# Kernel optimization log

Hardware: AMD Instinct MI355X
Metric: run time of the kernel (lower is better)

Reference implementation:

```python
import jax, jax.numpy as jnp
import numpy as np

VOCAB = 50000
EMB = 128
HID = 256
OUT = 1


def setup_inputs() -> dict:
    key = jax.random.key(0)
    ks = jax.random.split(key, 8)
    B, T = 256, 512
    s_emb = 1.0 / np.sqrt(EMB)
    s_hid = 1.0 / np.sqrt(HID)
    return {
        "x": jax.random.randint(ks[0], (B, T), 0, VOCAB, dtype=jnp.int32),
        "emb_table": jax.random.normal(ks[1], (VOCAB, EMB), dtype=jnp.float32),
        "W_ih": jax.random.uniform(ks[2], (4 * HID, EMB), jnp.float32, -s_hid, s_hid),
        "W_hh": jax.random.uniform(ks[3], (4 * HID, HID), jnp.float32, -s_hid, s_hid),
        "b_ih": jax.random.uniform(ks[4], (4 * HID,), jnp.float32, -s_hid, s_hid),
        "b_hh": jax.random.uniform(ks[5], (4 * HID,), jnp.float32, -s_hid, s_hid),
        "W_fc": jax.random.uniform(ks[6], (OUT, HID), jnp.float32, -s_hid, s_hid),
        "b_fc": jax.random.uniform(ks[7], (OUT,), jnp.float32, -s_hid, s_hid),
    }


def _lstm_last_hidden(embedded, W_ih, W_hh, b_ih, b_hh):
    # embedded: [B, T, E]; PyTorch gate order: i, f, g, o
    B = embedded.shape[0]
    H = W_hh.shape[1]
    # precompute input projections for all timesteps: [T, B, 4H]
    x_proj = jnp.einsum('bte,ge->tbg', embedded, W_ih) + b_ih + b_hh

    def step(carry, xp):
        h, c = carry
        gates = xp + h @ W_hh.T  # [B, 4H]
        i, f, g, o = jnp.split(gates, 4, axis=-1)
        i = jax.nn.sigmoid(i)
        f = jax.nn.sigmoid(f)
        g = jnp.tanh(g)
        o = jax.nn.sigmoid(o)
        c = f * c + i * g
        h = o * jnp.tanh(c)
        return (h, c), None

    h0 = jnp.zeros((B, H), embedded.dtype)
    c0 = jnp.zeros((B, H), embedded.dtype)
    (h_last, _), _ = jax.lax.scan(step, (h0, c0), x_proj)
    return h_last  # [B, H] == lstm_out[:, -1, :]


def reference(x, emb_table, W_ih, W_hh, b_ih, b_hh, W_fc, b_fc):
    embedded = emb_table[x]  # [B, T, E]
    h_last = _lstm_last_hidden(embedded, W_ih, W_hh, b_ih, b_hh)
    logits = h_last @ W_fc.T + b_fc  # [B, OUT]
    return jax.nn.sigmoid(logits)
```

## Files before the change

kernel.cpp:

```cpp
#include <hip/hip_runtime.h>
#include <hip/hip_bf16.h>
#include <stdint.h>

#define VOCAB 50000
#define EMB   128
#define HID   256
#define G4    1024
#define BATCH 256
#define SEQ   512
#define LOG2E 1.4426950408889634f

typedef __attribute__((ext_vector_type(8))) short bf16x8;
typedef __attribute__((ext_vector_type(4))) float f32x4;
typedef __attribute__((ext_vector_type(4))) int   i32x4;

__device__ __forceinline__ ushort f2bf(float f) {
  uint32_t u; __builtin_memcpy(&u, &f, 4);
  uint32_t r = (u + 0x7fffu + ((u >> 16) & 1u)) >> 16;
  return (ushort)r;
}
__device__ __forceinline__ float asf(uint32_t x) {
  float f; __builtin_memcpy(&f, &x, 4);
  return f;
}
__device__ __forceinline__ float rcp(float x) { return __builtin_amdgcn_rcpf(x); }
__device__ __forceinline__ float ex2(float x) { return __builtin_amdgcn_exp2f(x); }

#define WAIT_LGKM() asm volatile("s_waitcnt lgkmcnt(0)" ::: "memory")
#define RAW_BAR()  do { __builtin_amdgcn_sched_barrier(0); \
                        __builtin_amdgcn_s_barrier(); \
                        __builtin_amdgcn_sched_barrier(0); } while (0)

__global__ __launch_bounds__(256) void k_proj(
    const float* __restrict__ emb, const float* __restrict__ W_ih,
    const float* __restrict__ b_ih, const float* __restrict__ b_hh,
    ushort* __restrict__ proj) {
  const int lane = threadIdx.x & 63;
  const int wv = threadIdx.x >> 6;
  const int vbase = (blockIdx.x * 4 + wv) * 64;
  const int lm = lane & 15, lq = lane >> 4;
  const int nt0 = blockIdx.y * 32;

  bf16x8 A[4][4];
  #pragma unroll
  for (int mt = 0; mt < 4; ++mt) {
    int v = vbase + mt * 16 + lm;
    int vc = v < VOCAB ? v : 0;
    const float* rp = emb + (size_t)vc * EMB;
    #pragma unroll
    for (int kt = 0; kt < 4; ++kt) {
      const float* p = rp + kt * 32 + lq * 8;
      #pragma unroll
      for (int i = 0; i < 8; ++i) A[mt][kt][i] = (short)f2bf(p[i]);
    }
  }
  for (int ntl = 0; ntl < 32; ++ntl) {
    const int g = (nt0 + ntl) * 16 + lm;
    const int newcol = (g & 255) * 4 + (g >> 8);
    bf16x8 B[4];
    #pragma unroll
    for (int kt = 0; kt < 4; ++kt) {
      const float* p = W_ih + (size_t)g * EMB + kt * 32 + lq * 8;
      #pragma unroll
      for (int i = 0; i < 8; ++i) B[kt][i] = (short)f2bf(p[i]);
    }
    const float bias = b_ih[g] + b_hh[g];
    #pragma unroll
    for (int mt = 0; mt < 4; ++mt) {
      f32x4 acc = {0.f, 0.f, 0.f, 0.f};
      #pragma unroll
      for (int kt = 0; kt < 4; ++kt)
        acc = __builtin_amdgcn_mfma_f32_16x16x32_bf16(A[mt][kt], B[kt], acc, 0, 0, 0);
      #pragma unroll
      for (int r = 0; r < 4; ++r) {
        int row = vbase + mt * 16 + lq * 4 + r;
        if (row < VOCAB) proj[(size_t)row * G4 + newcol] = f2bf((acc[r] + bias) * LOG2E);
      }
    }
  }
}

__global__ __launch_bounds__(256) void k_w2(const float* __restrict__ Whh,
                                            int* __restrict__ W3) {
  const int t = blockIdx.x * 256 + threadIdx.x;
  const int lane = t & 63, c = t >> 6;
  const int kq = c & 15, wv = (c >> 4) & 7, v = c >> 7;
  const int gp = lane >> 5;
  const int j = wv * 32 + (lane & 31);
  const int g = gp * 2 + v;
  const float* src = Whh + (size_t)(g * 256 + j) * HID + kq * 16;
  unsigned d[4];
  #pragma unroll
  for (int e = 0; e < 4; ++e) {
    unsigned acc = 0;
    #pragma unroll
    for (int b = 0; b < 4; ++b) {
      int q = (int)rintf(src[e * 4 + b] * 2032.f);
      q = q > 127 ? 127 : (q < -127 ? -127 : q);
      acc |= ((unsigned)q & 0xffu) << (8 * b);
    }
    d[e] = acc;
  }
  i32x4 o = {(int)d[0], (int)d[1], (int)d[2], (int)d[3]};
  *(i32x4*)(W3 + (size_t)(c * 64 + lane) * 4) = o;
}

__global__ __launch_bounds__(512, 1) void k_lstm(
    const int* __restrict__ x, const ushort* __restrict__ proj,
    const int* __restrict__ W3, const float* __restrict__ W_fc,
    const float* __restrict__ b_fc, float* __restrict__ out) {
  __shared__ __align__(16) char hbuf[2][256];
  __shared__ __align__(16) int xlds[SEQ];
  __shared__ float red[8];

  const int tid = threadIdx.x;
  const int lane = tid & 63, wv = tid >> 6;
  const int gp = lane >> 5;
  const int j = wv * 32 + (lane & 31);
  const int b0 = blockIdx.x;
  const unsigned colb = (unsigned)(j * 4 + gp * 2) * 2u;

  i32x4 Wd0[16], Wd1[16];
  {
    const i32x4* wb = (const i32x4*)W3;
    #pragma unroll
    for (int kq = 0; kq < 16; ++kq) {
      Wd0[kq] = wb[(size_t)((0 * 8 + wv) * 16 + kq) * 64 + lane];
      Wd1[kq] = wb[(size_t)((1 * 8 + wv) * 16 + kq) * 64 + lane];
    }
    #pragma unroll
    for (int kq = 0; kq < 16; ++kq) {
      asm volatile("" : "+v"(Wd0[kq]));
      asm volatile("" : "+v"(Wd1[kq]));
    }
  }

  for (int i = tid; i < SEQ; i += 512) xlds[i] = x[b0 * SEQ + i];
  if (tid < 128) ((int*)hbuf)[tid] = 0;

  float c = 0.f, hl = 0.f;
  __syncthreads();

  const char* projb = (const char*)proj;
  unsigned xp0, xp1;
  xp0 = *(const unsigned*)(projb + (unsigned)xlds[0] * 2048u + colb);
  xp1 = *(const unsigned*)(projb + (unsigned)xlds[1] * 2048u + colb);

  const float S2 = LOG2E / 258064.f;

#define STEP(T, RB, WB, XP)                                                   \
  {                                                                           \
    int p0 = 0, p1 = 0, p2 = 0, p3 = 0;                    \
    int q0 = 0, q1 = 0, q2 = 0, q3 = 0;                    \
    _Pragma("unroll")                                                         \
    for (int kh = 0; kh < 2; ++kh) {                                          \
      i32x4 hq[8];                                                            \
      _Pragma("unroll")                                                       \
      for (int k8 = 0; k8 < 8; ++k8)                                          \
        hq[k8] = *(const i32x4*)(hbuf[RB] + (kh * 8 + k8) * 16);              \
      _Pragma("unroll")                                                       \
      for (int k8 = 0; k8 < 8; ++k8) {                                        \
        const int kq = kh * 8 + k8;                                           \
        p0 = __builtin_amdgcn_sdot4(hq[k8][0], Wd0[kq][0], p0, false);        \
        p1 = __builtin_amdgcn_sdot4(hq[k8][1], Wd0[kq][1], p1, false);        \
        p2 = __builtin_amdgcn_sdot4(hq[k8][2], Wd0[kq][2], p2, false);        \
        p3 = __builtin_amdgcn_sdot4(hq[k8][3], Wd0[kq][3], p3, false);        \
        q0 = __builtin_amdgcn_sdot4(hq[k8][0], Wd1[kq][0], q0, false);        \
        q1 = __builtin_amdgcn_sdot4(hq[k8][1], Wd1[kq][1], q1, false);        \
        q2 = __builtin_amdgcn_sdot4(hq[k8][2], Wd1[kq][2], q2, false);        \
        q3 = __builtin_amdgcn_sdot4(hq[k8][3], Wd1[kq][3], q3, false);        \
      }                                                                       \
    }                                                                         \
    int a0 = (p0 + p1) + (p2 + p3);                                           \
    int a1 = (q0 + q1) + (q2 + q3);                                           \
    float gv0 = (float)a0 * S2 + asf(XP << 16);                               \
    float gv1 = (float)a1 * S2 + asf(XP & 0xffff0000u);                       \
    float og0 = __shfl_xor(gv0, 32);                                          \
    float og1 = __shfl_xor(gv1, 32);                                          \
    float gi = gp ? og0 : gv0;                                                \
    float gf = gp ? og1 : gv1;                                                \
    float gg = gp ? gv0 : og0;                                                \
    float go = gp ? gv1 : og1;                                                \
    float si_ = rcp(1.f + ex2(-gi));                                          \
    float sf_ = rcp(1.f + ex2(-gf));                                          \
    float eg_ = ex2(gg + gg);                                                 \
    float tg_ = (eg_ - 1.f) * rcp(eg_ + 1.f);                                 \
    float so_ = rcp(1.f + ex2(-go));                                          \
    float cn_ = sf_ * c + si_ * tg_;                                          \
    c = cn_;                                                                  \
    float e2_ = ex2(cn_ * (2.f * LOG2E));                                     \
    float tc_ = 1.f - 2.f * rcp(e2_ + 1.f);                                   \
    float h_ = so_ * tc_;                                                     \
    hl = h_;                                                                  \
    if (gp == 0) hbuf[WB][j] = (char)(int)rintf(h_ * 127.f);                  \
    {                                                     \
      int t2_ = ((T) + 2 < SEQ) ? (T) + 2 : SEQ - 1;                          \
      XP = *(const unsigned*)(projb + (unsigned)xlds[t2_] * 2048u + colb);    \
    }                                                                         \
    WAIT_LGKM();                                                              \
    RAW_BAR();                                                                \
  }

  STEP(0, 0, 1, xp0);
  #pragma clang loop unroll(disable)
  for (int tt = 0; tt < 255; ++tt) {
    STEP(2 * tt + 1, 1, 0, xp1);
    STEP(2 * tt + 2, 0, 1, xp0);
  }
  STEP(511, 1, 0, xp1);

  float p = hl * W_fc[j];
  p += __shfl_xor(p, 1);
  p += __shfl_xor(p, 2);
  p += __shfl_xor(p, 4);
  p += __shfl_xor(p, 8);
  p += __shfl_xor(p, 16);
  if (lane == 0) red[wv] = p;
  __syncthreads();
  if (tid == 0) {
    float s = 0.f;
    #pragma unroll
    for (int w = 0; w < 8; ++w) s += red[w];
    s += b_fc[0];
    out[b0] = rcp(1.f + ex2(-s * LOG2E));
  }
}

extern "C" void kernel_launch(void* const* d_in, const int* in_sizes, int n_in,
                              void* d_out, int out_size, void* d_ws, size_t ws_size,
                              hipStream_t stream) {
  const int*   x    = (const int*)d_in[0];
  const float* emb  = (const float*)d_in[1];
  const float* W_ih = (const float*)d_in[2];
  const float* W_hh = (const float*)d_in[3];
  const float* b_ih = (const float*)d_in[4];
  const float* b_hh = (const float*)d_in[5];
  const float* W_fc = (const float*)d_in[6];
  const float* b_fc = (const float*)d_in[7];
  float* out = (float*)d_out;

  char* ws = (char*)d_ws;
  ushort* proj = (ushort*)ws;
  int*    W3   = (int*)(ws + 102400000);

  k_proj<<<dim3(196, 2), dim3(256), 0, stream>>>(emb, W_ih, b_ih, b_hh, proj);
  k_w2<<<dim3(64), dim3(256), 0, stream>>>(W_hh, W3);
  k_lstm<<<dim3(256), dim3(512), 0, stream>>>(x, proj, W3, W_fc, b_fc, out);
}
```

Baseline: 559.2 us.

## Split recurrent gate matvec between int8 MFMA and sdot4 paths

Gates g and o of the recurrent matvec now go through int8 MFMA (16x16x64) with weights held in AGPRs. Gates i and f stay on the sdot4 path, with K split across the two half-waves and combined by a shuffle. The W_hh quantization is split into two packing kernels with new layouts, and the projection load is widened to fetch all four gates per lane. The aim is to shorten the per-timestep serial dot-product latency by moving half the work onto the matrix cores. The cost is extra bpermutes and MFMA latency on the critical path, plus wasted MFMA rows because only one batch row is real.

```diff
diff --git a/kernel.cpp b/kernel.cpp
--- a/kernel.cpp
+++ b/kernel.cpp
@@ -13,6 +13,7 @@
 typedef __attribute__((ext_vector_type(8))) short bf16x8;
 typedef __attribute__((ext_vector_type(4))) float f32x4;
 typedef __attribute__((ext_vector_type(4))) int   i32x4;
+typedef __attribute__((ext_vector_type(2))) unsigned u32x2;
 
 __device__ __forceinline__ ushort f2bf(float f) {
   uint32_t u; __builtin_memcpy(&u, &f, 4);
@@ -81,14 +82,12 @@
 }
 
 __global__ __launch_bounds__(256) void k_w2(const float* __restrict__ Whh,
-                                            int* __restrict__ W3) {
+                                            int* __restrict__ W2) {
   const int t = blockIdx.x * 256 + threadIdx.x;
-  const int lane = t & 63, c = t >> 6;
-  const int kq = c & 15, wv = (c >> 4) & 7, v = c >> 7;
-  const int gp = lane >> 5;
-  const int j = wv * 32 + (lane & 31);
-  const int g = gp * 2 + v;
-  const float* src = Whh + (size_t)(g * 256 + j) * HID + kq * 16;
+  const int lane = t & 63, kc = (t >> 6) & 3, nt2 = (t >> 8) & 3, wv = (t >> 10) & 7;
+  const int grow = 512 + (nt2 >> 1) * 256 + wv * 32 + (nt2 & 1) * 16 + (lane & 15);
+  const int k0 = kc * 64 + (lane >> 4) * 16;
+  const float* src = Whh + (size_t)grow * HID + k0;
   unsigned d[4];
   #pragma unroll
   for (int e = 0; e < 4; ++e) {
@@ -102,37 +101,75 @@
     d[e] = acc;
   }
   i32x4 o = {(int)d[0], (int)d[1], (int)d[2], (int)d[3]};
-  *(i32x4*)(W3 + (size_t)(c * 64 + lane) * 4) = o;
+  *(i32x4*)(W2 + (size_t)t * 4) = o;
+}
+
+__global__ __launch_bounds__(256) void k_w3(const float* __restrict__ Whh,
+                                            int* __restrict__ W3) {
+  const int t = blockIdx.x * 256 + threadIdx.x;
+  const int lane = t & 63, n = (t >> 6) & 15, wv = t >> 10;
+  const int gate = n >> 3, kk = n & 7;
+  const int grow = gate * 256 + wv * 32 + (lane & 31);
+  const int k0 = (lane >> 5) * 128 + kk * 16;
+  const float* src = Whh + (size_t)grow * HID + k0;
+  unsigned d[4];
+  #pragma unroll
+  for (int e = 0; e < 4; ++e) {
+    unsigned acc = 0;
+    #pragma unroll
+    for (int b = 0; b < 4; ++b) {
+      int q = (int)rintf(src[e * 4 + b] * 2032.f);
+      q = q > 127 ? 127 : (q < -127 ? -127 : q);
+      acc |= ((unsigned)q & 0xffu) << (8 * b);
+    }
+    d[e] = acc;
+  }
+  i32x4 o = {(int)d[0], (int)d[1], (int)d[2], (int)d[3]};
+  *(i32x4*)(W3 + (size_t)t * 4) = o;
 }
 
 __global__ __launch_bounds__(512, 1) void k_lstm(
     const int* __restrict__ x, const ushort* __restrict__ proj,
-    const int* __restrict__ W3, const float* __restrict__ W_fc,
-    const float* __restrict__ b_fc, float* __restrict__ out) {
+    const int* __restrict__ W2, const int* __restrict__ W3,
+    const float* __restrict__ W_fc, const float* __restrict__ b_fc,
+    float* __restrict__ out) {
   __shared__ __align__(16) char hbuf[2][256];
   __shared__ __align__(16) int xlds[SEQ];
   __shared__ float red[8];
 
   const int tid = threadIdx.x;
   const int lane = tid & 63, wv = tid >> 6;
-  const int gp = lane >> 5;
-  const int j = wv * 32 + (lane & 31);
+  const int jl = lane & 31, kh = lane >> 5;
+  const int j = wv * 32 + jl;
+  const int js = (lane >> 4) & 1, lm = lane & 15;
+  const int lq = lane >> 4;
   const int b0 = blockIdx.x;
-  const unsigned colb = (unsigned)(j * 4 + gp * 2) * 2u;
-
-  i32x4 Wd0[16], Wd1[16];
+  const int bp = lm * 4;
+  const unsigned colb = (unsigned)j * 8u;
+
+  i32x4 Wf[4][4];
+  {
+    const i32x4* wb = (const i32x4*)W2;
+    #pragma unroll
+    for (int nt2 = 0; nt2 < 4; ++nt2)
+      #pragma unroll
+      for (int kc = 0; kc < 4; ++kc)
+        Wf[nt2][kc] = wb[((wv * 4 + nt2) * 4 + kc) * 64 + lane];
+    #pragma unroll
+    for (int nt2 = 0; nt2 < 4; ++nt2)
+      #pragma unroll
+      for (int kc = 0; kc < 4; ++kc)
+        asm volatile("" : "+a"(Wf[nt2][kc]));
+  }
+  i32x4 Wd[16];
   {
     const i32x4* wb = (const i32x4*)W3;
     #pragma unroll
-    for (int kq = 0; kq < 16; ++kq) {
-      Wd0[kq] = wb[(size_t)((0 * 8 + wv) * 16 + kq) * 64 + lane];
-      Wd1[kq] = wb[(size_t)((1 * 8 + wv) * 16 + kq) * 64 + lane];
-    }
-    #pragma unroll
-    for (int kq = 0; kq < 16; ++kq) {
-      asm volatile("" : "+v"(Wd0[kq]));
-      asm volatile("" : "+v"(Wd1[kq]));
-    }
+    for (int n = 0; n < 16; ++n)
+      Wd[n] = wb[(wv * 16 + n) * 64 + lane];
+    #pragma unroll
+    for (int n = 0; n < 16; ++n)
+      asm volatile("" : "+v"(Wd[n]));
   }
 
   for (int i = tid; i < SEQ; i += 512) xlds[i] = x[b0 * SEQ + i];
@@ -142,45 +179,60 @@
   __syncthreads();
 
   const char* projb = (const char*)proj;
-  unsigned xp0, xp1;
-  xp0 = *(const unsigned*)(projb + (unsigned)xlds[0] * 2048u + colb);
-  xp1 = *(const unsigned*)(projb + (unsigned)xlds[1] * 2048u + colb);
+  u32x2 xp0, xp1;
+  xp0 = *(const u32x2*)(projb + (unsigned)xlds[0] * 2048u + colb);
+  xp1 = *(const u32x2*)(projb + (unsigned)xlds[1] * 2048u + colb);
 
   const float S2 = LOG2E / 258064.f;
 
 #define STEP(T, RB, WB, XP)                                                   \
   {                                                                           \
-    int p0 = 0, p1 = 0, p2 = 0, p3 = 0;                    \
-    int q0 = 0, q1 = 0, q2 = 0, q3 = 0;                    \
+    const char* hb_ = hbuf[RB];                                               \
+    i32x4 A[4];                                             \
     _Pragma("unroll")                                                         \
-    for (int kh = 0; kh < 2; ++kh) {                                          \
-      i32x4 hq[8];                                                            \
+    for (int kc = 0; kc < 4; ++kc)                                            \
+      A[kc] = *(const i32x4*)(hb_ + kc * 64 + lq * 16);                       \
+    i32x4 hq[8];                                           \
+    _Pragma("unroll")                                                         \
+    for (int kk = 0; kk < 8; ++kk)                                            \
+      hq[kk] = *(const i32x4*)(hb_ + kh * 128 + kk * 16);                     \
+                                 \
+    i32x4 ag0 = {0,0,0,0}, ag1 = {0,0,0,0}, ao0 = {0,0,0,0}, ao1 = {0,0,0,0}; \
+    _Pragma("unroll")                                                         \
+    for (int kc = 0; kc < 4; ++kc) {                                          \
+      ag0 = __builtin_amdgcn_mfma_i32_16x16x64_i8(A[kc], Wf[0][kc], ag0, 0, 0, 0); \
+      ag1 = __builtin_amdgcn_mfma_i32_16x16x64_i8(A[kc], Wf[1][kc], ag1, 0, 0, 0); \
+      ao0 = __builtin_amdgcn_mfma_i32_16x16x64_i8(A[kc], Wf[2][kc], ao0, 0, 0, 0); \
+      ao1 = __builtin_amdgcn_mfma_i32_16x16x64_i8(A[kc], Wf[3][kc], ao1, 0, 0, 0); \
+    }                                                                         \
+              \
+    int pi0 = 0, pi1 = 0, pf0 = 0, pf1 = 0;                                   \
+    _Pragma("unroll")                                                         \
+    for (int kk = 0; kk < 8; ++kk) {                                          \
       _Pragma("unroll")                                                       \
-      for (int k8 = 0; k8 < 8; ++k8)                                          \
-        hq[k8] = *(const i32x4*)(hbuf[RB] + (kh * 8 + k8) * 16);              \
-      _Pragma("unroll")                                                       \
-      for (int k8 = 0; k8 < 8; ++k8) {                                        \
-        const int kq = kh * 8 + k8;                                           \
-        p0 = __builtin_amdgcn_sdot4(hq[k8][0], Wd0[kq][0], p0, false);        \
-        p1 = __builtin_amdgcn_sdot4(hq[k8][1], Wd0[kq][1], p1, false);        \
-        p2 = __builtin_amdgcn_sdot4(hq[k8][2], Wd0[kq][2], p2, false);        \
-        p3 = __builtin_amdgcn_sdot4(hq[k8][3], Wd0[kq][3], p3, false);        \
-        q0 = __builtin_amdgcn_sdot4(hq[k8][0], Wd1[kq][0], q0, false);        \
-        q1 = __builtin_amdgcn_sdot4(hq[k8][1], Wd1[kq][1], q1, false);        \
-        q2 = __builtin_amdgcn_sdot4(hq[k8][2], Wd1[kq][2], q2, false);        \
-        q3 = __builtin_amdgcn_sdot4(hq[k8][3], Wd1[kq][3], q3, false);        \
+      for (int e = 0; e < 4; ++e) {                                           \
+        if (kk & 1) {                                                         \
+          pi1 = __builtin_amdgcn_sdot4(hq[kk][e], Wd[kk][e], pi1, false);     \
+          pf1 = __builtin_amdgcn_sdot4(hq[kk][e], Wd[8 + kk][e], pf1, false); \
+        } else {                                                              \
+          pi0 = __builtin_amdgcn_sdot4(hq[kk][e], Wd[kk][e], pi0, false);     \
+          pf0 = __builtin_amdgcn_sdot4(hq[kk][e], Wd[8 + kk][e], pf0, false); \
+        }                                                                     \
       }                                                                       \
     }                                                                         \
-    int a0 = (p0 + p1) + (p2 + p3);                                           \
-    int a1 = (q0 + q1) + (q2 + q3);                                           \
-    float gv0 = (float)a0 * S2 + asf(XP << 16);                               \
-    float gv1 = (float)a1 * S2 + asf(XP & 0xffff0000u);                       \
-    float og0 = __shfl_xor(gv0, 32);                                          \
-    float og1 = __shfl_xor(gv1, 32);                                          \
-    float gi = gp ? og0 : gv0;                                                \
-    float gf = gp ? og1 : gv1;                                                \
-    float gg = gp ? gv0 : og0;                                                \
-    float go = gp ? gv1 : og1;                                                \
+    int ai = pi0 + pi1; ai += __shfl_xor(ai, 32);              \
+    int af = pf0 + pf1; af += __shfl_xor(af, 32);                             \
+                       \
+    int g0 = __builtin_amdgcn_ds_bpermute(bp, ag0[0]);                        \
+    int g1 = __builtin_amdgcn_ds_bpermute(bp, ag1[0]);                        \
+    int o0 = __builtin_amdgcn_ds_bpermute(bp, ao0[0]);                        \
+    int o1 = __builtin_amdgcn_ds_bpermute(bp, ao1[0]);                        \
+    int agv = js ? g1 : g0;                                                   \
+    int aov = js ? o1 : o0;                                                   \
+    float gi = (float)ai * S2 + asf(XP[0] << 16);                             \
+    float gf = (float)af * S2 + asf(XP[0] & 0xffff0000u);                     \
+    float gg = (float)agv * S2 + asf(XP[1] << 16);                            \
+    float go = (float)aov * S2 + asf(XP[1] & 0xffff0000u);                    \
     float si_ = rcp(1.f + ex2(-gi));                                          \
     float sf_ = rcp(1.f + ex2(-gf));                                          \
     float eg_ = ex2(gg + gg);                                                 \
@@ -192,10 +244,10 @@
     float tc_ = 1.f - 2.f * rcp(e2_ + 1.f);                                   \
     float h_ = so_ * tc_;                                                     \
     hl = h_;                                                                  \
-    if (gp == 0) hbuf[WB][j] = (char)(int)rintf(h_ * 127.f);                  \
-    {                                                     \
+    if (kh == 0) hbuf[WB][j] = (char)(int)rintf(h_ * 127.f);                  \
+    {                                                         \
       int t2_ = ((T) + 2 < SEQ) ? (T) + 2 : SEQ - 1;                          \
-      XP = *(const unsigned*)(projb + (unsigned)xlds[t2_] * 2048u + colb);    \
+      XP = *(const u32x2*)(projb + (unsigned)xlds[t2_] * 2048u + colb);       \
     }                                                                         \
     WAIT_LGKM();                                                              \
     RAW_BAR();                                                                \
@@ -241,9 +293,11 @@
 
   char* ws = (char*)d_ws;
   ushort* proj = (ushort*)ws;
-  int*    W3   = (int*)(ws + 102400000);
+  int*    W2   = (int*)(ws + 102400000);
+  int*    W3   = (int*)(ws + 102531072);
 
   k_proj<<<dim3(196, 2), dim3(256), 0, stream>>>(emb, W_ih, b_ih, b_hh, proj);
-  k_w2<<<dim3(64), dim3(256), 0, stream>>>(W_hh, W3);
-  k_lstm<<<dim3(256), dim3(512), 0, stream>>>(x, proj, W3, W_fc, b_fc, out);
-}
+  k_w2<<<dim3(32), dim3(256), 0, stream>>>(W_hh, W2);
+  k_w3<<<dim3(32), dim3(256), 0, stream>>>(W_hh, W3);
+  k_lstm<<<dim3(256), dim3(512), 0, stream>>>(x, proj, W2, W3, W_fc, b_fc, out);
+}
```

After: 647.4 us. +15.8%, slower.

## Give each LSTM thread all four gates of one hidden unit, halving the block

Applied to the files above, without the earlier changes.

The recurrent kernel now runs 256 threads per block, and each thread holds the int8 W_hh rows for all four gates of one hidden unit in registers. This drops the cross-half shuffle exchange and doubles the per-thread dot-product work per step. A new prep kernel converts W_ih to bf16 once, scales it and the bias by log2e, and k_proj then loads bf16 vectors directly instead of converting in its inner loop. The cost is about 256 VGPRs of weights per thread and a longer serial sdot chain per timestep, with fewer waves available to hide latency.

```diff
diff --git a/kernel.cpp b/kernel.cpp
--- a/kernel.cpp
+++ b/kernel.cpp
@@ -13,6 +13,7 @@
 typedef __attribute__((ext_vector_type(8))) short bf16x8;
 typedef __attribute__((ext_vector_type(4))) float f32x4;
 typedef __attribute__((ext_vector_type(4))) int   i32x4;
+typedef __attribute__((ext_vector_type(2))) unsigned u32x2;
 
 __device__ __forceinline__ ushort f2bf(float f) {
   uint32_t u; __builtin_memcpy(&u, &f, 4);
@@ -31,10 +32,18 @@
                         __builtin_amdgcn_s_barrier(); \
                         __builtin_amdgcn_sched_barrier(0); } while (0)
 
+__global__ __launch_bounds__(256) void k_prep(
+    const float* __restrict__ W_ih, const float* __restrict__ b_ih,
+    const float* __restrict__ b_hh, ushort* __restrict__ Wihb,
+    float* __restrict__ bvec) {
+  int t = blockIdx.x * 256 + threadIdx.x;
+  Wihb[t] = f2bf(W_ih[t] * LOG2E);
+  if (t < G4) bvec[t] = (b_ih[t] + b_hh[t]) * LOG2E;
+}
+
 __global__ __launch_bounds__(256) void k_proj(
-    const float* __restrict__ emb, const float* __restrict__ W_ih,
-    const float* __restrict__ b_ih, const float* __restrict__ b_hh,
-    ushort* __restrict__ proj) {
+    const float* __restrict__ emb, const ushort* __restrict__ Wihb,
+    const float* __restrict__ bvec, ushort* __restrict__ proj) {
   const int lane = threadIdx.x & 63;
   const int wv = threadIdx.x >> 6;
   const int vbase = (blockIdx.x * 4 + wv) * 64;
@@ -59,12 +68,9 @@
     const int newcol = (g & 255) * 4 + (g >> 8);
     bf16x8 B[4];
     #pragma unroll
-    for (int kt = 0; kt < 4; ++kt) {
-      const float* p = W_ih + (size_t)g * EMB + kt * 32 + lq * 8;
-      #pragma unroll
-      for (int i = 0; i < 8; ++i) B[kt][i] = (short)f2bf(p[i]);
-    }
-    const float bias = b_ih[g] + b_hh[g];
+    for (int kt = 0; kt < 4; ++kt)
+      B[kt] = *(const bf16x8*)(Wihb + (size_t)g * EMB + kt * 32 + lq * 8);
+    const float bias = bvec[g];
     #pragma unroll
     for (int mt = 0; mt < 4; ++mt) {
       f32x4 acc = {0.f, 0.f, 0.f, 0.f};
@@ -74,21 +80,19 @@
       #pragma unroll
       for (int r = 0; r < 4; ++r) {
         int row = vbase + mt * 16 + lq * 4 + r;
-        if (row < VOCAB) proj[(size_t)row * G4 + newcol] = f2bf((acc[r] + bias) * LOG2E);
+        if (row < VOCAB) proj[(size_t)row * G4 + newcol] = f2bf(acc[r] + bias);
       }
     }
   }
 }
 
-__global__ __launch_bounds__(256) void k_w2(const float* __restrict__ Whh,
+__global__ __launch_bounds__(256) void k_w3(const float* __restrict__ Whh,
                                             int* __restrict__ W3) {
   const int t = blockIdx.x * 256 + threadIdx.x;
-  const int lane = t & 63, c = t >> 6;
-  const int kq = c & 15, wv = (c >> 4) & 7, v = c >> 7;
-  const int gp = lane >> 5;
-  const int j = wv * 32 + (lane & 31);
-  const int g = gp * 2 + v;
-  const float* src = Whh + (size_t)(g * 256 + j) * HID + kq * 16;
+  const int lane = t & 63, kk = (t >> 6) & 15, gate = (t >> 10) & 3, wv = t >> 12;
+  const int grow = gate * 256 + wv * 64 + lane;
+  const int k0 = kk * 16;
+  const float* src = Whh + (size_t)grow * HID + k0;
   unsigned d[4];
   #pragma unroll
   for (int e = 0; e < 4; ++e) {
@@ -102,85 +106,71 @@
     d[e] = acc;
   }
   i32x4 o = {(int)d[0], (int)d[1], (int)d[2], (int)d[3]};
-  *(i32x4*)(W3 + (size_t)(c * 64 + lane) * 4) = o;
-}
-
-__global__ __launch_bounds__(512, 1) void k_lstm(
+  *(i32x4*)(W3 + (size_t)t * 4) = o;
+}
+
+__global__ __launch_bounds__(256, 1) void k_lstm(
     const int* __restrict__ x, const ushort* __restrict__ proj,
     const int* __restrict__ W3, const float* __restrict__ W_fc,
     const float* __restrict__ b_fc, float* __restrict__ out) {
   __shared__ __align__(16) char hbuf[2][256];
   __shared__ __align__(16) int xlds[SEQ];
-  __shared__ float red[8];
+  __shared__ float red[4];
 
   const int tid = threadIdx.x;
   const int lane = tid & 63, wv = tid >> 6;
-  const int gp = lane >> 5;
-  const int j = wv * 32 + (lane & 31);
   const int b0 = blockIdx.x;
-  const unsigned colb = (unsigned)(j * 4 + gp * 2) * 2u;
-
-  i32x4 Wd0[16], Wd1[16];
+  const unsigned colb = (unsigned)tid * 8u;
+
+  i32x4 Wd[4][16];
   {
     const i32x4* wb = (const i32x4*)W3;
     #pragma unroll
-    for (int kq = 0; kq < 16; ++kq) {
-      Wd0[kq] = wb[(size_t)((0 * 8 + wv) * 16 + kq) * 64 + lane];
-      Wd1[kq] = wb[(size_t)((1 * 8 + wv) * 16 + kq) * 64 + lane];
-    }
-    #pragma unroll
-    for (int kq = 0; kq < 16; ++kq) {
-      asm volatile("" : "+v"(Wd0[kq]));
-      asm volatile("" : "+v"(Wd1[kq]));
-    }
-  }
-
-  for (int i = tid; i < SEQ; i += 512) xlds[i] = x[b0 * SEQ + i];
+    for (int gate = 0; gate < 4; ++gate)
+      #pragma unroll
+      for (int kk = 0; kk < 16; ++kk)
+        Wd[gate][kk] = wb[(size_t)(((wv * 4 + gate) * 16) + kk) * 64 + lane];
+    #pragma unroll
+    for (int gate = 0; gate < 4; ++gate)
+      #pragma unroll
+      for (int kk = 0; kk < 16; ++kk)
+        asm volatile("" : "+v"(Wd[gate][kk]));
+  }
+
+  for (int i = tid; i < SEQ; i += 256) xlds[i] = x[b0 * SEQ + i];
   if (tid < 128) ((int*)hbuf)[tid] = 0;
 
   float c = 0.f, hl = 0.f;
   __syncthreads();
 
   const char* projb = (const char*)proj;
-  unsigned xp0, xp1;
-  xp0 = *(const unsigned*)(projb + (unsigned)xlds[0] * 2048u + colb);
-  xp1 = *(const unsigned*)(projb + (unsigned)xlds[1] * 2048u + colb);
+  u32x2 xp0, xp1;
+  xp0 = *(const u32x2*)(projb + (unsigned)xlds[0] * 2048u + colb);
+  xp1 = *(const u32x2*)(projb + (unsigned)xlds[1] * 2048u + colb);
 
   const float S2 = LOG2E / 258064.f;
 
 #define STEP(T, RB, WB, XP)                                                   \
   {                                                                           \
-    int p0 = 0, p1 = 0, p2 = 0, p3 = 0;                    \
-    int q0 = 0, q1 = 0, q2 = 0, q3 = 0;                    \
+    i32x4 hq[16];                                      \
     _Pragma("unroll")                                                         \
-    for (int kh = 0; kh < 2; ++kh) {                                          \
-      i32x4 hq[8];                                                            \
+    for (int kk = 0; kk < 16; ++kk)                                           \
+      hq[kk] = *(const i32x4*)(hbuf[RB] + kk * 16);                           \
+    int ai = 0, af = 0, ag = 0, ao = 0;                     \
+    _Pragma("unroll")                                                         \
+    for (int kk = 0; kk < 16; ++kk) {                                         \
       _Pragma("unroll")                                                       \
-      for (int k8 = 0; k8 < 8; ++k8)                                          \
-        hq[k8] = *(const i32x4*)(hbuf[RB] + (kh * 8 + k8) * 16);              \
-      _Pragma("unroll")                                                       \
-      for (int k8 = 0; k8 < 8; ++k8) {                                        \
-        const int kq = kh * 8 + k8;                                           \
-        p0 = __builtin_amdgcn_sdot4(hq[k8][0], Wd0[kq][0], p0, false);        \
-        p1 = __builtin_amdgcn_sdot4(hq[k8][1], Wd0[kq][1], p1, false);        \
-        p2 = __builtin_amdgcn_sdot4(hq[k8][2], Wd0[kq][2], p2, false);        \
-        p3 = __builtin_amdgcn_sdot4(hq[k8][3], Wd0[kq][3], p3, false);        \
-        q0 = __builtin_amdgcn_sdot4(hq[k8][0], Wd1[kq][0], q0, false);        \
-        q1 = __builtin_amdgcn_sdot4(hq[k8][1], Wd1[kq][1], q1, false);        \
-        q2 = __builtin_amdgcn_sdot4(hq[k8][2], Wd1[kq][2], q2, false);        \
-        q3 = __builtin_amdgcn_sdot4(hq[k8][3], Wd1[kq][3], q3, false);        \
+      for (int e = 0; e < 4; ++e) {                                           \
+        ai = __builtin_amdgcn_sdot4(hq[kk][e], Wd[0][kk][e], ai, false);      \
+        af = __builtin_amdgcn_sdot4(hq[kk][e], Wd[1][kk][e], af, false);      \
+        ag = __builtin_amdgcn_sdot4(hq[kk][e], Wd[2][kk][e], ag, false);      \
+        ao = __builtin_amdgcn_sdot4(hq[kk][e], Wd[3][kk][e], ao, false);      \
       }                                                                       \
     }                                                                         \
-    int a0 = (p0 + p1) + (p2 + p3);                                           \
-    int a1 = (q0 + q1) + (q2 + q3);                                           \
-    float gv0 = (float)a0 * S2 + asf(XP << 16);                               \
-    float gv1 = (float)a1 * S2 + asf(XP & 0xffff0000u);                       \
-    float og0 = __shfl_xor(gv0, 32);                                          \
-    float og1 = __shfl_xor(gv1, 32);                                          \
-    float gi = gp ? og0 : gv0;                                                \
-    float gf = gp ? og1 : gv1;                                                \
-    float gg = gp ? gv0 : og0;                                                \
-    float go = gp ? gv1 : og1;                                                \
+    float gi = (float)ai * S2 + asf(XP[0] << 16);                             \
+    float gf = (float)af * S2 + asf(XP[0] & 0xffff0000u);                     \
+    float gg = (float)ag * S2 + asf(XP[1] << 16);                             \
+    float go = (float)ao * S2 + asf(XP[1] & 0xffff0000u);                     \
     float si_ = rcp(1.f + ex2(-gi));                                          \
     float sf_ = rcp(1.f + ex2(-gf));                                          \
     float eg_ = ex2(gg + gg);                                                 \
@@ -189,13 +179,13 @@
     float cn_ = sf_ * c + si_ * tg_;                                          \
     c = cn_;                                                                  \
     float e2_ = ex2(cn_ * (2.f * LOG2E));                                     \
-    float tc_ = 1.f - 2.f * rcp(e2_ + 1.f);                                   \
+    float tc_ = 1.f - 2.f * rcp(e2_ + 1.f);                      \
     float h_ = so_ * tc_;                                                     \
     hl = h_;                                                                  \
-    if (gp == 0) hbuf[WB][j] = (char)(int)rintf(h_ * 127.f);                  \
-    {                                                     \
+    hbuf[WB][tid] = (char)(int)rintf(h_ * 127.f);                             \
+    {                                                         \
       int t2_ = ((T) + 2 < SEQ) ? (T) + 2 : SEQ - 1;                          \
-      XP = *(const unsigned*)(projb + (unsigned)xlds[t2_] * 2048u + colb);    \
+      XP = *(const u32x2*)(projb + (unsigned)xlds[t2_] * 2048u + colb);       \
     }                                                                         \
     WAIT_LGKM();                                                              \
     RAW_BAR();                                                                \
@@ -209,19 +199,17 @@
   }
   STEP(511, 1, 0, xp1);
 
-  float p = hl * W_fc[j];
+  float p = hl * W_fc[tid];
   p += __shfl_xor(p, 1);
   p += __shfl_xor(p, 2);
   p += __shfl_xor(p, 4);
   p += __shfl_xor(p, 8);
   p += __shfl_xor(p, 16);
+  p += __shfl_xor(p, 32);
   if (lane == 0) red[wv] = p;
   __syncthreads();
   if (tid == 0) {
-    float s = 0.f;
-    #pragma unroll
-    for (int w = 0; w < 8; ++w) s += red[w];
-    s += b_fc[0];
+    float s = red[0] + red[1] + red[2] + red[3] + b_fc[0];
     out[b0] = rcp(1.f + ex2(-s * LOG2E));
   }
 }
@@ -242,8 +230,11 @@
   char* ws = (char*)d_ws;
   ushort* proj = (ushort*)ws;
   int*    W3   = (int*)(ws + 102400000);
-
-  k_proj<<<dim3(196, 2), dim3(256), 0, stream>>>(emb, W_ih, b_ih, b_hh, proj);
-  k_w2<<<dim3(64), dim3(256), 0, stream>>>(W_hh, W3);
-  k_lstm<<<dim3(256), dim3(512), 0, stream>>>(x, proj, W3, W_fc, b_fc, out);
-}
+  ushort* Wihb = (ushort*)(ws + 102662144);
+  float*  bvec = (float*)(ws + 102924288);
+
+  k_prep<<<dim3(512), dim3(256), 0, stream>>>(W_ih, b_ih, b_hh, Wihb, bvec);
+  k_w3<<<dim3(64), dim3(256), 0, stream>>>(W_hh, W3);
+  k_proj<<<dim3(196, 2), dim3(256), 0, stream>>>(emb, Wihb, bvec, proj);
+  k_lstm<<<dim3(256), dim3(256), 0, stream>>>(x, proj, W3, W_fc, b_fc, out);
+}
```

Measured after the change: 853.9 us. +52.7%, slower.
